# Kernel optimization log

Hardware: AMD Instinct MI355X
Metric: run time of the kernel (lower is better)

## Reference

```python
import jax, jax.numpy as jnp
import numpy as np

B, I, D = 256, 1152, 8   # batch, input_num_capsule, input_dim_vector
C, O = 10, 16            # num_capsule, dim_vector
NUM_ROUTING = 3
EPS = 1e-7


def squash(s, axis=-1):
    # v = ||s||^2 / (1 + ||s||^2) * s / ||s||
    n2 = jnp.sum(jnp.square(s), axis=axis, keepdims=True)
    return (n2 / (1.0 + n2)) * s / jnp.sqrt(n2 + EPS)


def setup_inputs() -> dict:
    key = jax.random.key(0)
    kx, kw = jax.random.split(key)
    x = jax.random.normal(kx, (B, I, D), dtype=jnp.float32)
    W = jax.random.normal(kw, (I, C, D, O), dtype=jnp.float32) * 0.05
    return {"x": x, "W": W}


def reference(x, W):
    # inputs_hat[b,i,c,o] = sum_d x[b,i,d] * W[i,c,d,o]
    # (the original tf.scan over batch of per-sample batch_dots == this einsum)
    inputs_hat = jnp.einsum('bid,icdo->bico', x, W)  # [B,I,C,O]

    bias = jnp.zeros((1, I, C, 1), dtype=x.dtype)    # routing logits
    outputs = None
    for r in range(NUM_ROUTING):
        c = jax.nn.softmax(bias, axis=2)             # softmax over num_capsule
        s = jnp.sum(c[..., None].squeeze(-1) * inputs_hat, axis=1, keepdims=True)  # [B,1,C,O]
        outputs = squash(s, axis=-1)                 # [B,1,C,O]
        if r != NUM_ROUTING - 1:
            bias = bias + jnp.sum(inputs_hat * outputs, axis=-1, keepdims=False)[..., None].squeeze(-1)[..., None]
    return outputs.reshape(B, C, O)
```

## Files before the change

kernel.cpp:

```cpp
#include <hip/hip_runtime.h>
#include <hip/hip_bf16.h>
#include <math.h>


#define B_ 256
#define I_ 1152
#define D_ 8
#define C_ 10
#define O_ 16
#define CO_ (C_*O_)
#define EPS_ 1e-7f

#define IC1 16
#define NIC1 (I_/IC1)
#define BT 16
#define NBT (B_/BT)
#define T1 320
#define IC3 128
#define NIC3 (I_/IC3)
#define T3 320

__global__ __launch_bounds__(T1) void k1_hat(
    const float* __restrict__ x,
    const float* __restrict__ W,
    __hip_bfloat16* __restrict__ hat,
    float* __restrict__ sPart1)
{
    __shared__ float xs[BT * IC1 * D_];
    __shared__ float sred[BT][CO_];
    const int tid = threadIdx.x;
    const int ic = blockIdx.x, bt = blockIdx.y;
    const int i0 = ic * IC1, b0 = bt * BT;

    for (int j = tid; j < BT * IC1 * D_ / 4; j += T1) {
        const int bb = j >> 5, r = j & 31;
        ((float4*)xs)[j] =
            *(const float4*)&x[(((size_t)(b0 + bb)) * I_ + i0) * D_ + r * 4];
    }
    __syncthreads();

    const int ig = tid / 80, r = tid % 80;
    const int c = r / 8, o2 = r % 8;

    float2 acc[BT];
    #pragma unroll
    for (int bb = 0; bb < BT; ++bb) acc[bb] = make_float2(0.0f, 0.0f);

    const float2* W2 = (const float2*)W;

    for (int k = 0; k < IC1 / 4; ++k) {
        const int il = ig * (IC1 / 4) + k;
        const int i = i0 + il;
        float2 wv[D_];
        const float2* wp = W2 + ((size_t)i * C_ + c) * (D_ * O_ / 2) + o2;
        #pragma unroll
        for (int d = 0; d < D_; ++d) wv[d] = wp[d * (O_ / 2)];
        #pragma unroll
        for (int bb = 0; bb < BT; ++bb) {
            const float4* xp4 = (const float4*)&xs[(bb * IC1 + il) * D_];
            const float4 xa = xp4[0];
            const float4 xb = xp4[1];
            const float xv[D_] = {xa.x, xa.y, xa.z, xa.w, xb.x, xb.y, xb.z, xb.w};
            float h0 = 0.0f, h1 = 0.0f;
            #pragma unroll
            for (int d = 0; d < D_; ++d) {
                h0 = fmaf(xv[d], wv[d].x, h0);
                h1 = fmaf(xv[d], wv[d].y, h1);
            }
            acc[bb].x += h0; acc[bb].y += h1;
            *(__hip_bfloat162*)&hat[((size_t)(b0 + bb) * I_ + i) * CO_ + c * O_ + o2 * 2] =
                __float22bfloat162_rn(make_float2(h0, h1));
        }
    }

    if (ig == 0) {
        #pragma unroll
        for (int bb = 0; bb < BT; ++bb) {
            sred[bb][c * O_ + o2 * 2]     = acc[bb].x;
            sred[bb][c * O_ + o2 * 2 + 1] = acc[bb].y;
        }
    }
    __syncthreads();
    #pragma unroll
    for (int g = 1; g < 4; ++g) {
        if (ig == g) {
            #pragma unroll
            for (int bb = 0; bb < BT; ++bb) {
                sred[bb][c * O_ + o2 * 2]     += acc[bb].x;
                sred[bb][c * O_ + o2 * 2 + 1] += acc[bb].y;
            }
        }
        __syncthreads();
    }
    if (tid < CO_) {
        for (int bb = 0; bb < BT; ++bb)
            sPart1[((size_t)ic * B_ + (b0 + bb)) * CO_ + tid] = sred[bb][tid];
    }
}

__device__ __forceinline__ void route_body(
    const __hip_bfloat16* __restrict__ hat, const float* vr,
    float* __restrict__ sPartR, int ic, int b, int il, int c, int tid)
{
    __shared__ float pb[32][C_];
    __shared__ float sr[32][CO_ + 4];
    const int i0 = ic * IC3;

    float sacc[O_];
    #pragma unroll
    for (int o = 0; o < O_; ++o) sacc[o] = 0.0f;

    for (int sb = 0; sb < IC3 / 32; ++sb) {
        const int i = i0 + sb * 32 + il;
        const uint4* hp = (const uint4*)&hat[((size_t)b * I_ + i) * CO_ + c * O_];
        const uint4 ha = hp[0], hb = hp[1];
        float hf[O_];
        {
            const unsigned u[8] = {ha.x, ha.y, ha.z, ha.w, hb.x, hb.y, hb.z, hb.w};
            #pragma unroll
            for (int q = 0; q < 8; ++q) {
                hf[2 * q]     = __uint_as_float(u[q] << 16);
                hf[2 * q + 1] = __uint_as_float(u[q] & 0xffff0000u);
            }
        }
        float p = 0.0f;
        #pragma unroll
        for (int o = 0; o < O_; ++o) p = fmaf(hf[o], vr[o], p);
        pb[il][c] = p;
        __syncthreads();
        float pv[C_];
        #pragma unroll
        for (int q = 0; q < C_; ++q) pv[q] = pb[il][q];
        float m = pv[0];
        #pragma unroll
        for (int q = 1; q < C_; ++q) m = fmaxf(m, pv[q]);
        float sum = 0.0f;
        #pragma unroll
        for (int q = 0; q < C_; ++q) sum += __expf(pv[q] - m);
        const float route = __expf(p - m) * __builtin_amdgcn_rcpf(sum);
        #pragma unroll
        for (int o = 0; o < O_; ++o) sacc[o] = fmaf(route, hf[o], sacc[o]);
        __syncthreads();
    }

    #pragma unroll
    for (int o = 0; o < O_; ++o) sr[il][c * O_ + o] = sacc[o];
    __syncthreads();
    if (tid < CO_) {
        float s = 0.0f;
        #pragma unroll
        for (int k = 0; k < 32; ++k) s += sr[k][tid];
        sPartR[((size_t)ic * B_ + b) * CO_ + tid] = s;
    }
}

__global__ __launch_bounds__(T3) void k_route2(
    const __hip_bfloat16* __restrict__ hat,
    const float* __restrict__ veff,
    float* __restrict__ sPartR)
{
    const int tid = threadIdx.x;
    const int il = tid / C_, c = tid % C_;
    const int ic = blockIdx.x, b = blockIdx.y;
    float vr[O_];
    #pragma unroll
    for (int o = 0; o < O_; ++o) vr[o] = veff[(size_t)b * CO_ + c * O_ + o];
    route_body(hat, vr, sPartR, ic, b, il, c, tid);
}

__global__ __launch_bounds__(T3) void k_route3(
    const __hip_bfloat16* __restrict__ hat,
    const float* __restrict__ veff1,
    const float* __restrict__ sPartR1,
    float* __restrict__ sPartR2)
{
    __shared__ float veffs[CO_];
    const int tid = threadIdx.x;
    const int il = tid / C_, c = tid % C_;
    const int ic = blockIdx.x, b = blockIdx.y;

    if (tid < CO_) {
        float s = 0.0f;
        #pragma unroll
        for (int k = 0; k < NIC3; ++k)
            s += sPartR1[((size_t)k * B_ + b) * CO_ + tid];
        float n2 = s * s;
        n2 += __shfl_xor(n2, 1);
        n2 += __shfl_xor(n2, 2);
        n2 += __shfl_xor(n2, 4);
        n2 += __shfl_xor(n2, 8);
        const float sc = n2 / ((1.0f + n2) * sqrtf(n2 + EPS_));
        veffs[tid] = veff1[(size_t)b * CO_ + tid] + s * sc;
    }
    __syncthreads();

    float vr[O_];
    #pragma unroll
    for (int o = 0; o < O_; ++o) vr[o] = veffs[c * O_ + o];
    route_body(hat, vr, sPartR2, ic, b, il, c, tid);
}

__global__ __launch_bounds__(640) void k_squash(
    const float* __restrict__ sPart,
    int nchunk, float scale,
    const float* __restrict__ prev,
    float* __restrict__ dst)
{
    __shared__ float red[4][CO_];
    const int b = blockIdx.x, tid = threadIdx.x;
    const int q = tid / CO_;
    const int co = tid % CO_;
    float s = 0.0f;
    for (int k = q; k < nchunk; k += 4)
        s += sPart[((size_t)k * B_ + b) * CO_ + co];
    red[q][co] = s;
    __syncthreads();
    if (tid < CO_) {
        s = (red[0][co] + red[1][co]) + (red[2][co] + red[3][co]);
        s *= scale;
        float n2 = s * s;
        n2 += __shfl_xor(n2, 1);
        n2 += __shfl_xor(n2, 2);
        n2 += __shfl_xor(n2, 4);
        n2 += __shfl_xor(n2, 8);
        const float sc = n2 / ((1.0f + n2) * sqrtf(n2 + EPS_));
        const float v = s * sc;
        dst[(size_t)b * CO_ + co] = (prev ? prev[(size_t)b * CO_ + co] : 0.0f) + v;
    }
}

#define THREADS 640
#define ILG 8
#define SUBI 4
#define CHUNK (ILG*SUBI)
#define NITER (I_/CHUNK)

__global__ __launch_bounds__(THREADS) void capsule_routing_kernel(
    const float* __restrict__ x, const float* __restrict__ W,
    float* __restrict__ out)
{
    __shared__ float bias[I_ * C_];
    __shared__ float spart[ILG][C_ * O_];
    __shared__ float sv[C_ * O_];
    __shared__ float vv[C_ * O_];
    __shared__ float ech[CHUNK][C_];
    __shared__ float scale[C_];

    const int b   = blockIdx.x;
    const int tid = threadIdx.x;
    for (int j = tid; j < I_ * C_; j += THREADS) bias[j] = 0.0f;
    const int il = tid / 80;
    const int rr = tid % 80;
    const int c  = rr / 8;
    const int o2 = rr % 8;
    const int o0 = o2 * 2;
    const float* xb = x + (size_t)b * I_ * D_;
    const float2* W2 = (const float2*)W;
    __syncthreads();
    {
        float acc0 = 0.0f, acc1 = 0.0f;
        for (int it = 0; it < NITER; ++it) {
            #pragma unroll
            for (int sub = 0; sub < SUBI; ++sub) {
                const int i = it * CHUNK + sub * ILG + il;
                const float* xi = xb + i * D_;
                const float2* wp = W2 + (i * C_ + c) * (D_ * O_ / 2) + o2;
                float h0 = 0.0f, h1 = 0.0f;
                #pragma unroll
                for (int d = 0; d < D_; ++d) {
                    float2 w = wp[d * (O_ / 2)];
                    float xv = xi[d];
                    h0 = fmaf(xv, w.x, h0);
                    h1 = fmaf(xv, w.y, h1);
                }
                acc0 += h0; acc1 += h1;
            }
        }
        spart[il][c * O_ + o0]     = acc0;
        spart[il][c * O_ + o0 + 1] = acc1;
    }
    __syncthreads();
    if (tid < C_ * O_) {
        float s = 0.0f;
        #pragma unroll
        for (int k = 0; k < ILG; ++k) s += spart[k][tid];
        sv[tid] = s * (1.0f / C_);
    }
    __syncthreads();
    if (tid < C_) {
        float n2 = 0.0f;
        #pragma unroll
        for (int o = 0; o < O_; ++o) { float t = sv[tid * O_ + o]; n2 = fmaf(t, t, n2); }
        scale[tid] = n2 / ((1.0f + n2) * sqrtf(n2 + EPS_));
    }
    __syncthreads();
    if (tid < C_ * O_) vv[tid] = sv[tid] * scale[tid / O_];
    __syncthreads();
    for (int pass = 1; pass < 3; ++pass) {
        float sa0 = 0.0f, sa1 = 0.0f;
        for (int it = 0; it < NITER; ++it) {
            float h0s[SUBI], h1s[SUBI];
            const float v0 = vv[c * O_ + o0];
            const float v1 = vv[c * O_ + o0 + 1];
            #pragma unroll
            for (int sub = 0; sub < SUBI; ++sub) {
                const int i = it * CHUNK + sub * ILG + il;
                const float* xi = xb + i * D_;
                const float2* wp = W2 + (i * C_ + c) * (D_ * O_ / 2) + o2;
                float h0 = 0.0f, h1 = 0.0f;
                #pragma unroll
                for (int d = 0; d < D_; ++d) {
                    float2 w = wp[d * (O_ / 2)];
                    float xv = xi[d];
                    h0 = fmaf(xv, w.x, h0);
                    h1 = fmaf(xv, w.y, h1);
                }
                h0s[sub] = h0; h1s[sub] = h1;
                float p = h0 * v0 + h1 * v1;
                p += __shfl_xor(p, 1);
                p += __shfl_xor(p, 2);
                p += __shfl_xor(p, 4);
                if (o2 == 0) bias[i * C_ + c] += p;
            }
            __syncthreads();
            if (tid < CHUNK * C_) {
                const int il2 = tid / C_, cc = tid % C_;
                const int i = it * CHUNK + il2;
                float m = -1e30f;
                #pragma unroll
                for (int k = 0; k < C_; ++k) m = fmaxf(m, bias[i * C_ + k]);
                ech[il2][cc] = __expf(bias[i * C_ + cc] - m);
            }
            __syncthreads();
            #pragma unroll
            for (int sub = 0; sub < SUBI; ++sub) {
                const int icx = sub * ILG + il;
                float sum = 0.0f;
                #pragma unroll
                for (int k = 0; k < C_; ++k) sum += ech[icx][k];
                const float route = ech[icx][c] / sum;
                sa0 = fmaf(route, h0s[sub], sa0);
                sa1 = fmaf(route, h1s[sub], sa1);
            }
            __syncthreads();
        }
        spart[il][c * O_ + o0]     = sa0;
        spart[il][c * O_ + o0 + 1] = sa1;
        __syncthreads();
        if (tid < C_ * O_) {
            float s = 0.0f;
            #pragma unroll
            for (int k = 0; k < ILG; ++k) s += spart[k][tid];
            sv[tid] = s;
        }
        __syncthreads();
        if (tid < C_) {
            float n2 = 0.0f;
            #pragma unroll
            for (int o = 0; o < O_; ++o) { float t = sv[tid * O_ + o]; n2 = fmaf(t, t, n2); }
            scale[tid] = n2 / ((1.0f + n2) * sqrtf(n2 + EPS_));
        }
        __syncthreads();
        if (tid < C_ * O_) vv[tid] = sv[tid] * scale[tid / O_];
        __syncthreads();
    }
    if (tid < C_ * O_) out[(size_t)b * C_ * O_ + tid] = vv[tid];
}

extern "C" void kernel_launch(void* const* d_in, const int* in_sizes, int n_in,
                              void* d_out, int out_size, void* d_ws, size_t ws_size,
                              hipStream_t stream) {
    (void)in_sizes; (void)n_in; (void)out_size;
    const float* x = (const float*)d_in[0];
    const float* W = (const float*)d_in[1];
    float* out = (float*)d_out;

    const size_t hat_b  = (size_t)B_ * I_ * CO_ * sizeof(__hip_bfloat16);
    const size_t sp1_b  = (size_t)NIC1 * B_ * CO_ * sizeof(float);
    const size_t spr_b  = (size_t)NIC3 * B_ * CO_ * sizeof(float);
    const size_t v_b    = (size_t)B_ * CO_ * sizeof(float);
    const size_t need   = hat_b + sp1_b + 2 * spr_b + v_b;

    if (ws_size >= need) {
        char* p = (char*)d_ws;
        __hip_bfloat16* hat = (__hip_bfloat16*)p;  p += hat_b;
        float* sPart1  = (float*)p;                p += sp1_b;
        float* sPartR1 = (float*)p;                p += spr_b;
        float* sPartR2 = (float*)p;                p += spr_b;
        float* veff1   = (float*)p;

        k1_hat<<<dim3(NIC1, NBT), T1, 0, stream>>>(x, W, hat, sPart1);
        k_squash<<<B_, 640, 0, stream>>>(sPart1, NIC1, 1.0f / C_, nullptr, veff1);
        k_route2<<<dim3(NIC3, B_), T3, 0, stream>>>(hat, veff1, sPartR1);
        k_route3<<<dim3(NIC3, B_), T3, 0, stream>>>(hat, veff1, sPartR1, sPartR2);
        k_squash<<<B_, 640, 0, stream>>>(sPartR2, NIC3, 1.0f, nullptr, out);
    } else {
        capsule_routing_kernel<<<B_, THREADS, 0, stream>>>(x, W, out);
    }
}
```

Before: 76.67 us.

## Fuse squash and both routing iterations into one per-batch kernel

```diff
diff --git a/kernel.cpp b/kernel.cpp
--- a/kernel.cpp
+++ b/kernel.cpp
@@ -16,9 +16,8 @@
 #define BT 16
 #define NBT (B_/BT)
 #define T1 320
-#define IC3 128
-#define NIC3 (I_/IC3)
-#define T3 320
+#define TRA 640
+#define NBATCH (I_/64)
 
 __global__ __launch_bounds__(T1) void k1_hat(
     const float* __restrict__ x,
@@ -98,134 +97,116 @@
     }
 }
 
-__device__ __forceinline__ void route_body(
-    const __hip_bfloat16* __restrict__ hat, const float* vr,
-    float* __restrict__ sPartR, int ic, int b, int il, int c, int tid)
+__global__ __launch_bounds__(TRA) void k_route_all(
+    const __hip_bfloat16* __restrict__ hat,
+    const float* __restrict__ sPart1,
+    float* __restrict__ out)
 {
-    __shared__ float pb[32][C_];
-    __shared__ float sr[32][CO_ + 4];
-    const int i0 = ic * IC3;
-
-    float sacc[O_];
-    #pragma unroll
-    for (int o = 0; o < O_; ++o) sacc[o] = 0.0f;
-
-    for (int sb = 0; sb < IC3 / 32; ++sb) {
-        const int i = i0 + sb * 32 + il;
-        const uint4* hp = (const uint4*)&hat[((size_t)b * I_ + i) * CO_ + c * O_];
-        const uint4 ha = hp[0], hb = hp[1];
-        float hf[O_];
-        {
-            const unsigned u[8] = {ha.x, ha.y, ha.z, ha.w, hb.x, hb.y, hb.z, hb.w};
-            #pragma unroll
-            for (int q = 0; q < 8; ++q) {
-                hf[2 * q]     = __uint_as_float(u[q] << 16);
-                hf[2 * q + 1] = __uint_as_float(u[q] & 0xffff0000u);
-            }
-        }
-        float p = 0.0f;
-        #pragma unroll
-        for (int o = 0; o < O_; ++o) p = fmaf(hf[o], vr[o], p);
-        pb[il][c] = p;
-        __syncthreads();
-        float pv[C_];
-        #pragma unroll
-        for (int q = 0; q < C_; ++q) pv[q] = pb[il][q];
-        float m = pv[0];
-        #pragma unroll
-        for (int q = 1; q < C_; ++q) m = fmaxf(m, pv[q]);
-        float sum = 0.0f;
-        #pragma unroll
-        for (int q = 0; q < C_; ++q) sum += __expf(pv[q] - m);
-        const float route = __expf(p - m) * __builtin_amdgcn_rcpf(sum);
-        #pragma unroll
-        for (int o = 0; o < O_; ++o) sacc[o] = fmaf(route, hf[o], sacc[o]);
-        __syncthreads();
-    }
-
-    #pragma unroll
-    for (int o = 0; o < O_; ++o) sr[il][c * O_ + o] = sacc[o];
-    __syncthreads();
-    if (tid < CO_) {
-        float s = 0.0f;
-        #pragma unroll
-        for (int k = 0; k < 32; ++k) s += sr[k][tid];
-        sPartR[((size_t)ic * B_ + b) * CO_ + tid] = s;
-    }
-}
-
-__global__ __launch_bounds__(T3) void k_route2(
-    const __hip_bfloat16* __restrict__ hat,
-    const float* __restrict__ veff,
-    float* __restrict__ sPartR)
-{
-    const int tid = threadIdx.x;
-    const int il = tid / C_, c = tid % C_;
-    const int ic = blockIdx.x, b = blockIdx.y;
-    float vr[O_];
-    #pragma unroll
-    for (int o = 0; o < O_; ++o) vr[o] = veff[(size_t)b * CO_ + c * O_ + o];
-    route_body(hat, vr, sPartR, ic, b, il, c, tid);
-}
-
-__global__ __launch_bounds__(T3) void k_route3(
-    const __hip_bfloat16* __restrict__ hat,
-    const float* __restrict__ veff1,
-    const float* __restrict__ sPartR1,
-    float* __restrict__ sPartR2)
-{
+    __shared__ float pb[2][64][C_];
+    __shared__ float sr[64][CO_ + 4];
+    __shared__ float red4[4][CO_];
     __shared__ float veffs[CO_];
     const int tid = threadIdx.x;
     const int il = tid / C_, c = tid % C_;
-    const int ic = blockIdx.x, b = blockIdx.y;
-
+    const int b = blockIdx.x;
+    const int q = tid / CO_;
+    const int co = tid % CO_;
+
+    {
+        float s = 0.0f;
+        #pragma unroll 2
+        for (int j = 0; j < NIC1 / 4; ++j)
+            s += sPart1[((size_t)(q * (NIC1 / 4) + j) * B_ + b) * CO_ + co];
+        red4[q][co] = s;
+    }
+    __syncthreads();
     if (tid < CO_) {
-        float s = 0.0f;
-        #pragma unroll
-        for (int k = 0; k < NIC3; ++k)
-            s += sPartR1[((size_t)k * B_ + b) * CO_ + tid];
+        float s = ((red4[0][tid] + red4[1][tid]) + (red4[2][tid] + red4[3][tid]))
+                  * (1.0f / C_);
         float n2 = s * s;
         n2 += __shfl_xor(n2, 1);
         n2 += __shfl_xor(n2, 2);
         n2 += __shfl_xor(n2, 4);
         n2 += __shfl_xor(n2, 8);
         const float sc = n2 / ((1.0f + n2) * sqrtf(n2 + EPS_));
-        veffs[tid] = veff1[(size_t)b * CO_ + tid] + s * sc;
-    }
-    __syncthreads();
-
-    float vr[O_];
-    #pragma unroll
-    for (int o = 0; o < O_; ++o) vr[o] = veffs[c * O_ + o];
-    route_body(hat, vr, sPartR2, ic, b, il, c, tid);
-}
-
-__global__ __launch_bounds__(640) void k_squash(
-    const float* __restrict__ sPart,
-    int nchunk, float scale,
-    const float* __restrict__ prev,
-    float* __restrict__ dst)
-{
-    __shared__ float red[4][CO_];
-    const int b = blockIdx.x, tid = threadIdx.x;
-    const int q = tid / CO_;
-    const int co = tid % CO_;
-    float s = 0.0f;
-    for (int k = q; k < nchunk; k += 4)
-        s += sPart[((size_t)k * B_ + b) * CO_ + co];
-    red[q][co] = s;
-    __syncthreads();
-    if (tid < CO_) {
-        s = (red[0][co] + red[1][co]) + (red[2][co] + red[3][co]);
-        s *= scale;
-        float n2 = s * s;
-        n2 += __shfl_xor(n2, 1);
-        n2 += __shfl_xor(n2, 2);
-        n2 += __shfl_xor(n2, 4);
-        n2 += __shfl_xor(n2, 8);
-        const float sc = n2 / ((1.0f + n2) * sqrtf(n2 + EPS_));
-        const float v = s * sc;
-        dst[(size_t)b * CO_ + co] = (prev ? prev[(size_t)b * CO_ + co] : 0.0f) + v;
+        veffs[tid] = s * sc;
+    }
+    __syncthreads();
+
+    const size_t baseB = (size_t)b * I_;
+
+    for (int round = 0; round < 2; ++round) {
+        float vr[O_];
+        #pragma unroll
+        for (int o = 0; o < O_; ++o) vr[o] = veffs[c * O_ + o];
+        float sacc[O_];
+        #pragma unroll
+        for (int o = 0; o < O_; ++o) sacc[o] = 0.0f;
+
+        uint4 ha, hb2, han, hbn;
+        {
+            const uint4* p0 = (const uint4*)&hat[(baseB + il) * CO_ + c * O_];
+            ha = p0[0]; hb2 = p0[1];
+        }
+        for (int batch = 0; batch < NBATCH; ++batch) {
+            if (batch < NBATCH - 1) {
+                const uint4* pn = (const uint4*)
+                    &hat[(baseB + (batch + 1) * 64 + il) * CO_ + c * O_];
+                han = pn[0]; hbn = pn[1];
+            }
+            float hf[O_];
+            {
+                const unsigned u[8] = {ha.x, ha.y, ha.z, ha.w,
+                                       hb2.x, hb2.y, hb2.z, hb2.w};
+                #pragma unroll
+                for (int t = 0; t < 8; ++t) {
+                    hf[2 * t]     = __uint_as_float(u[t] << 16);
+                    hf[2 * t + 1] = __uint_as_float(u[t] & 0xffff0000u);
+                }
+            }
+            float p = 0.0f;
+            #pragma unroll
+            for (int o = 0; o < O_; ++o) p = fmaf(hf[o], vr[o], p);
+            pb[batch & 1][il][c] = p;
+            __syncthreads();
+            float pv[C_];
+            #pragma unroll
+            for (int qq = 0; qq < C_; ++qq) pv[qq] = pb[batch & 1][il][qq];
+            float m = pv[0];
+            #pragma unroll
+            for (int qq = 1; qq < C_; ++qq) m = fmaxf(m, pv[qq]);
+            float sum = 0.0f;
+            #pragma unroll
+            for (int qq = 0; qq < C_; ++qq) sum += __expf(pv[qq] - m);
+            const float route = __expf(p - m) * __builtin_amdgcn_rcpf(sum);
+            #pragma unroll
+            for (int o = 0; o < O_; ++o) sacc[o] = fmaf(route, hf[o], sacc[o]);
+            ha = han; hb2 = hbn;
+        }
+
+        #pragma unroll
+        for (int o = 0; o < O_; ++o) sr[il][c * O_ + o] = sacc[o];
+        __syncthreads();
+        {
+            float s = 0.0f;
+            #pragma unroll
+            for (int j = 0; j < 16; ++j) s += sr[q * 16 + j][co];
+            red4[q][co] = s;
+        }
+        __syncthreads();
+        if (tid < CO_) {
+            float s = (red4[0][tid] + red4[1][tid]) + (red4[2][tid] + red4[3][tid]);
+            float n2 = s * s;
+            n2 += __shfl_xor(n2, 1);
+            n2 += __shfl_xor(n2, 2);
+            n2 += __shfl_xor(n2, 4);
+            n2 += __shfl_xor(n2, 8);
+            const float sc = n2 / ((1.0f + n2) * sqrtf(n2 + EPS_));
+            const float v = s * sc;
+            if (round == 0) veffs[tid] += v;
+            else out[(size_t)b * CO_ + tid] = v;
+        }
+        __syncthreads();
     }
 }
 
@@ -377,23 +358,15 @@
 
     const size_t hat_b  = (size_t)B_ * I_ * CO_ * sizeof(__hip_bfloat16);
     const size_t sp1_b  = (size_t)NIC1 * B_ * CO_ * sizeof(float);
-    const size_t spr_b  = (size_t)NIC3 * B_ * CO_ * sizeof(float);
-    const size_t v_b    = (size_t)B_ * CO_ * sizeof(float);
-    const size_t need   = hat_b + sp1_b + 2 * spr_b + v_b;
+    const size_t need   = hat_b + sp1_b;
 
     if (ws_size >= need) {
         char* p = (char*)d_ws;
         __hip_bfloat16* hat = (__hip_bfloat16*)p;  p += hat_b;
-        float* sPart1  = (float*)p;                p += sp1_b;
-        float* sPartR1 = (float*)p;                p += spr_b;
-        float* sPartR2 = (float*)p;                p += spr_b;
-        float* veff1   = (float*)p;
+        float* sPart1 = (float*)p;
 
         k1_hat<<<dim3(NIC1, NBT), T1, 0, stream>>>(x, W, hat, sPart1);
-        k_squash<<<B_, 640, 0, stream>>>(sPart1, NIC1, 1.0f / C_, nullptr, veff1);
-        k_route2<<<dim3(NIC3, B_), T3, 0, stream>>>(hat, veff1, sPartR1);
-        k_route3<<<dim3(NIC3, B_), T3, 0, stream>>>(hat, veff1, sPartR1, sPartR2);
-        k_squash<<<B_, 640, 0, stream>>>(sPartR2, NIC3, 1.0f, nullptr, out);
+        k_route_all<<<B_, TRA, 0, stream>>>(hat, sPart1, out);
     } else {
         capsule_routing_kernel<<<B_, THREADS, 0, stream>>>(x, W, out);
     }
```

Measured after the change: 61.74 us, median of 2. -19.5%, faster.
